# Kernel optimization log

Hardware: AMD Instinct MI355X
Metric: run time of the kernel (lower is better)

Reference implementation:

```python
import jax, jax.numpy as jnp
import numpy as np

NUM_EXPERTS = 64
TOP_K = 2
AUX_COEF = 0.01
Z_COEF = 0.001
INIT_STD = 0.02


def setup_inputs() -> dict:
    key = jax.random.key(0)
    k1, k2 = jax.random.split(key)
    B, S, D = 4, 4096, 2048
    x = jax.random.normal(k1, (B, S, D), dtype=jnp.float32)
    gate_w = jax.random.normal(k2, (NUM_EXPERTS, D), dtype=jnp.float32) * INIT_STD
    return {"x": x, "gate_w": gate_w}


def reference(x, gate_w):
    B, S, D = x.shape
    E, K = NUM_EXPERTS, TOP_K
    # gate linear: (B,S,D) @ (D,E) -> (B,S,E), cast to fp32 like .float()
    logits = jnp.einsum('bsd,ed->bse', x, gate_w).astype(jnp.float32)
    weights = jax.nn.softmax(logits, axis=-1)
    top_weights, top_indices = jax.lax.top_k(weights, K)
    top_weights = top_weights / jnp.sum(top_weights, axis=-1, keepdims=True)
    # load-balance aux loss (training branch)
    flat_idx = top_indices.reshape(-1)
    tokens_per_expert = jax.ops.segment_sum(
        jnp.ones_like(flat_idx, dtype=jnp.float32), flat_idx, num_segments=E)
    f = tokens_per_expert / (B * S * K)
    P = jnp.mean(weights, axis=(0, 1))
    balance_loss = E * jnp.sum(f * P)
    z_loss = jnp.mean(jnp.square(jax.nn.logsumexp(logits, axis=-1)))
    aux_loss = AUX_COEF * balance_loss + Z_COEF * z_loss
    return top_indices, top_weights, aux_loss
```

## Files before the change

### kernel.cpp

```cpp
#include <hip/hip_runtime.h>
#include <math.h>

#define NTOK 16384
#define DDIM 2048
#define NEXP 64
#define NKQ 16
#define KSLICE 128
#define TPB 64

typedef __attribute__((ext_vector_type(8))) short bf16x8;
typedef __attribute__((ext_vector_type(4))) float f32x4;


__device__ __forceinline__ void split3pk(float a, float b,
                                         unsigned &H, unsigned &M, unsigned &L) {
    asm("v_cvt_pk_bf16_f32 %0, %1, %2" : "=v"(H) : "v"(a), "v"(b));
    float ra = a - __builtin_bit_cast(float, H << 16);
    float rb = b - __builtin_bit_cast(float, H & 0xffff0000u);
    asm("v_cvt_pk_bf16_f32 %0, %1, %2" : "=v"(M) : "v"(ra), "v"(rb));
    float sa = ra - __builtin_bit_cast(float, M << 16);
    float sb = rb - __builtin_bit_cast(float, M & 0xffff0000u);
    asm("v_cvt_pk_bf16_f32 %0, %1, %2" : "=v"(L) : "v"(sa), "v"(sb));
}

__device__ __forceinline__ void keepf(float4 &v) {
    asm volatile("" : "+v"(v.x), "+v"(v.y), "+v"(v.z), "+v"(v.w));
}

__global__ void k_wpack(const float* __restrict__ gw, unsigned short* __restrict__ wp,
                        float* __restrict__ aux) {
    if (blockIdx.x == 0 && threadIdx.x < 132) aux[threadIdx.x] = 0.f;
    int idx = blockIdx.x * 256 + threadIdx.x;
    int lane = idx & 63;
    int ks   = (idx >> 6) & 63;
    int eg   = idx >> 12;
    int e  = eg * 16 + (lane & 15);
    int k0 = ks * 32 + (lane >> 4) * 8;
    const float* src = gw + (size_t)e * DDIM + k0;
    uint4 H, M, L;
    split3pk(src[0], src[1], H.x, M.x, L.x);
    split3pk(src[2], src[3], H.y, M.y, L.y);
    split3pk(src[4], src[5], H.z, M.z, L.z);
    split3pk(src[6], src[7], H.w, M.w, L.w);
    size_t fb = ((size_t)ks * 12 + eg * 3) * 512 + lane * 8;
    *(uint4*)(wp + fb)        = H;
    *(uint4*)(wp + fb + 512)  = M;
    *(uint4*)(wp + fb + 1024) = L;
}

__global__ __launch_bounds__(256, 2)
void k_gemm(const float* __restrict__ x, const unsigned short* __restrict__ wp,
            float* __restrict__ part) {
    __shared__ __align__(16) char Ws[49152];

    const int tid  = threadIdx.x;
    const int kq   = blockIdx.x & 15;
    const int tok0 = (blockIdx.x >> 4) * TPB;
    const int lane = tid & 63;
    const int wvu  = __builtin_amdgcn_readfirstlane(tid >> 6);
    const int tau  = lane & 15;
    const int kap  = lane >> 4;

    {
        const char* wsrc = (const char*)wp + (size_t)kq * 49152;
        #pragma unroll
        for (int r = 0; r < 12; ++r) {
            const char* g = wsrc + (size_t)(r * 256 + tid) * 16;
            char* l = Ws + (size_t)(r * 256 + wvu * 64) * 16;
            __builtin_amdgcn_global_load_lds(
                (const __attribute__((address_space(1))) void*)g,
                (__attribute__((address_space(3))) void*)l, 16, 0, 0);
        }
    }

    const float* xb = x + (size_t)(tok0 + wvu * 16 + tau) * DDIM
                        + kq * KSLICE + kap * 8;
    float4 x0a = *(const float4*)(xb);
    float4 x0b = *(const float4*)(xb + 4);
    float4 x1a = *(const float4*)(xb + 32);
    float4 x1b = *(const float4*)(xb + 36);
    float4 x2a = *(const float4*)(xb + 64);
    float4 x2b = *(const float4*)(xb + 68);
    float4 x3a = *(const float4*)(xb + 96);
    float4 x3b = *(const float4*)(xb + 100);
    keepf(x0a); keepf(x0b); keepf(x1a); keepf(x1b);
    keepf(x2a); keepf(x2b); keepf(x3a); keepf(x3b);

    __syncthreads();

    f32x4 acc[4];
    #pragma unroll
    for (int eg = 0; eg < 4; ++eg) acc[eg] = (f32x4){0.f, 0.f, 0.f, 0.f};

    #pragma unroll
    for (int ks = 0; ks < 4; ++ks) {
        float4 a = (ks == 0) ? x0a : (ks == 1) ? x1a : (ks == 2) ? x2a : x3a;
        float4 b = (ks == 0) ? x0b : (ks == 1) ? x1b : (ks == 2) ? x2b : x3b;
        uint4 Ah, Am, Al;
        split3pk(a.x, a.y, Ah.x, Am.x, Al.x);
        split3pk(a.z, a.w, Ah.y, Am.y, Al.y);
        split3pk(b.x, b.y, Ah.z, Am.z, Al.z);
        split3pk(b.z, b.w, Ah.w, Am.w, Al.w);
        bf16x8 Ahv = __builtin_bit_cast(bf16x8, Ah);
        bf16x8 Amv = __builtin_bit_cast(bf16x8, Am);
        bf16x8 Alv = __builtin_bit_cast(bf16x8, Al);

        #pragma unroll
        for (int eg = 0; eg < 4; ++eg) {
            const char* wb = Ws + ks * 12288 + eg * 3072 + lane * 16;
            bf16x8 Bh = *(const bf16x8*)(wb);
            bf16x8 Bm = *(const bf16x8*)(wb + 1024);
            bf16x8 Bl = *(const bf16x8*)(wb + 2048);
            acc[eg] = __builtin_amdgcn_mfma_f32_16x16x32_bf16(Ahv, Bh, acc[eg], 0, 0, 0);
            acc[eg] = __builtin_amdgcn_mfma_f32_16x16x32_bf16(Ahv, Bm, acc[eg], 0, 0, 0);
            acc[eg] = __builtin_amdgcn_mfma_f32_16x16x32_bf16(Amv, Bh, acc[eg], 0, 0, 0);
            acc[eg] = __builtin_amdgcn_mfma_f32_16x16x32_bf16(Ahv, Bl, acc[eg], 0, 0, 0);
            acc[eg] = __builtin_amdgcn_mfma_f32_16x16x32_bf16(Alv, Bh, acc[eg], 0, 0, 0);
            acc[eg] = __builtin_amdgcn_mfma_f32_16x16x32_bf16(Amv, Bm, acc[eg], 0, 0, 0);
        }
    }

    float* pb = part + ((size_t)kq * NTOK + tok0 + wvu * 16) * 64;
    #pragma unroll
    for (int eg = 0; eg < 4; ++eg)
        #pragma unroll
        for (int j = 0; j < 4; ++j)
            pb[(kap * 4 + j) * 64 + eg * 16 + tau] = acc[eg][j];
}

__global__ __launch_bounds__(256, 2)
void k_reduce(const float* __restrict__ part, float* __restrict__ out,
              float* __restrict__ gcnt, float* __restrict__ gP,
              float* __restrict__ gz) {
    __shared__ float Ps[NEXP], Cnt[NEXP], Zs;
    const int tid = threadIdx.x;
    if (tid < NEXP) { Ps[tid] = 0.f; Cnt[tid] = 0.f; }
    if (tid == 0) Zs = 0.f;
    __syncthreads();

    const int lane = tid & 63;
    const int wv   = tid >> 6;
    const int g    = lane >> 4;
    const int s    = lane & 15;
    const int t    = blockIdx.x * 16 + wv * 4 + g;
    const int e4   = s * 4;

    f32x4 a = {0.f, 0.f, 0.f, 0.f};
    #pragma unroll
    for (int q = 0; q < NKQ; ++q) {
        const f32x4 v = *(const f32x4*)(part + ((size_t)q * NTOK + t) * 64 + e4);
        a[0] += v[0]; a[1] += v[1]; a[2] += v[2]; a[3] += v[3];
    }

    float m1 = a[0], m2 = -INFINITY;
    int   i1 = e4,   i2 = NEXP;
    #pragma unroll
    for (int j = 1; j < 4; ++j) {
        float v = a[j]; int idx = e4 + j;
        if (v > m1)      { m2 = m1; i2 = i1; m1 = v; i1 = idx; }
        else if (v > m2) { m2 = v;  i2 = idx; }
    }
    #pragma unroll
    for (int off = 1; off < 16; off <<= 1) {
        float n1 = __shfl_xor(m1, off, 16);
        int   j1 = __shfl_xor(i1, off, 16);
        float n2 = __shfl_xor(m2, off, 16);
        int   j2 = __shfl_xor(i2, off, 16);
        bool pwin = (n1 > m1) || (n1 == m1 && j1 < i1);
        float w1 = pwin ? n1 : m1;  int wi1 = pwin ? j1 : i1;
        float c  = pwin ? m1 : n1;  int ci  = pwin ? i1 : j1;
        float ws = pwin ? n2 : m2;  int wsi = pwin ? j2 : i2;
        bool csec = (c > ws) || (c == ws && ci < wsi);
        m1 = w1; i1 = wi1;
        m2 = csec ? c : ws; i2 = csec ? ci : wsi;
    }

    float ex0 = expf(a[0] - m1), ex1 = expf(a[1] - m1);
    float ex2 = expf(a[2] - m1), ex3 = expf(a[3] - m1);
    float sum = (ex0 + ex1) + (ex2 + ex3);
    #pragma unroll
    for (int off = 1; off < 16; off <<= 1) sum += __shfl_xor(sum, off, 16);

    float inv = 1.f / sum;
    atomicAdd(&Ps[e4 + 0], ex0 * inv);
    atomicAdd(&Ps[e4 + 1], ex1 * inv);
    atomicAdd(&Ps[e4 + 2], ex2 * inv);
    atomicAdd(&Ps[e4 + 3], ex3 * inv);

    if (s == 0) {
        float s2  = expf(m2 - m1);
        float w1v = 1.f / (1.f + s2);
        ((float2*)out)[t]              = make_float2((float)i1, (float)i2);
        ((float2*)(out + 2 * NTOK))[t] = make_float2(w1v, s2 * w1v);
        atomicAdd(&Cnt[i1], 1.f);
        atomicAdd(&Cnt[i2], 1.f);
        float lse = m1 + logf(sum);
        atomicAdd(&Zs, lse * lse);
    }
    __syncthreads();

    if (tid < NEXP) {
        atomicAdd(&gcnt[tid], Cnt[tid]);
        atomicAdd(&gP[tid],   Ps[tid]);
    }
    if (tid == 0) atomicAdd(gz, Zs);
}

__global__ void k_final(const float* __restrict__ ws, float* __restrict__ out) {
    int lane = threadIdx.x;
    float v = ws[lane] * ws[64 + lane];
    #pragma unroll
    for (int off = 32; off > 0; off >>= 1) v += __shfl_xor(v, off);
    if (lane == 0) {
        float bal = 64.f * v / (32768.f * 16384.f);
        float z   = ws[128] / 16384.f;
        out[4 * NTOK] = 0.01f * bal + 0.001f * z;
    }
}

extern "C" void kernel_launch(void* const* d_in, const int* in_sizes, int n_in,
                              void* d_out, int out_size, void* d_ws, size_t ws_size,
                              hipStream_t stream) {
    const float* x  = (const float*)d_in[0];
    const float* gw = (const float*)d_in[1];
    float* out = (float*)d_out;
    float* wsf = (float*)d_ws;
    unsigned short* wp = (unsigned short*)((char*)d_ws + 1024);
    float* part = (float*)((char*)d_ws + (1 << 20));

    k_wpack<<<64, 256, 0, stream>>>(gw, wp, wsf);
    k_gemm<<<NKQ * (NTOK / TPB), 256, 0, stream>>>(x, wp, part);
    k_reduce<<<NTOK / 16, 256, 0, stream>>>(part, out, wsf, wsf + 64, wsf + 128);
    k_final<<<1, 64, 0, stream>>>(wsf, out);
}
```

Measured before the change: 79.15 us.

## Fuse weight packing into GEMM and final loss into reduce kernel

Drops the separate weight-packing kernel. Each GEMM block now loads its fp32 gate-weight slice, splits it into three bf16 parts and writes them straight to LDS. The final aux-loss kernel is folded into the reduce kernel through a last-block-done atomic counter. Together this removes two kernel launches and the packed-weight round trip through global memory, at the cost of every GEMM block redoing the bf16 split on its slice and more VALU work before the MFMA loop.

```diff
diff --git a/kernel.cpp b/kernel.cpp
--- a/kernel.cpp
+++ b/kernel.cpp
@@ -27,30 +27,9 @@
     asm volatile("" : "+v"(v.x), "+v"(v.y), "+v"(v.z), "+v"(v.w));
 }
 
-__global__ void k_wpack(const float* __restrict__ gw, unsigned short* __restrict__ wp,
-                        float* __restrict__ aux) {
-    if (blockIdx.x == 0 && threadIdx.x < 132) aux[threadIdx.x] = 0.f;
-    int idx = blockIdx.x * 256 + threadIdx.x;
-    int lane = idx & 63;
-    int ks   = (idx >> 6) & 63;
-    int eg   = idx >> 12;
-    int e  = eg * 16 + (lane & 15);
-    int k0 = ks * 32 + (lane >> 4) * 8;
-    const float* src = gw + (size_t)e * DDIM + k0;
-    uint4 H, M, L;
-    split3pk(src[0], src[1], H.x, M.x, L.x);
-    split3pk(src[2], src[3], H.y, M.y, L.y);
-    split3pk(src[4], src[5], H.z, M.z, L.z);
-    split3pk(src[6], src[7], H.w, M.w, L.w);
-    size_t fb = ((size_t)ks * 12 + eg * 3) * 512 + lane * 8;
-    *(uint4*)(wp + fb)        = H;
-    *(uint4*)(wp + fb + 512)  = M;
-    *(uint4*)(wp + fb + 1024) = L;
-}
-
 __global__ __launch_bounds__(256, 2)
-void k_gemm(const float* __restrict__ x, const unsigned short* __restrict__ wp,
-            float* __restrict__ part) {
+void k_gemm(const float* __restrict__ x, const float* __restrict__ gw,
+            float* __restrict__ part, float* __restrict__ aux) {
     __shared__ __align__(16) char Ws[49152];
 
     const int tid  = threadIdx.x;
@@ -61,17 +40,7 @@
     const int tau  = lane & 15;
     const int kap  = lane >> 4;
 
-    {
-        const char* wsrc = (const char*)wp + (size_t)kq * 49152;
-        #pragma unroll
-        for (int r = 0; r < 12; ++r) {
-            const char* g = wsrc + (size_t)(r * 256 + tid) * 16;
-            char* l = Ws + (size_t)(r * 256 + wvu * 64) * 16;
-            __builtin_amdgcn_global_load_lds(
-                (const __attribute__((address_space(1))) void*)g,
-                (__attribute__((address_space(3))) void*)l, 16, 0, 0);
-        }
-    }
+    if (blockIdx.x == 0 && tid < 136) aux[tid] = 0.f;
 
     const float* xb = x + (size_t)(tok0 + wvu * 16 + tau) * DDIM
                         + kq * KSLICE + kap * 8;
@@ -83,9 +52,31 @@
     float4 x2b = *(const float4*)(xb + 68);
     float4 x3a = *(const float4*)(xb + 96);
     float4 x3b = *(const float4*)(xb + 100);
+
+    {
+        const int e  = tid >> 2;
+        const int ks = tid & 3;
+        const int eg = e >> 4;
+        const float* gsrc = gw + (size_t)e * DDIM + kq * KSLICE + ks * 32;
+        char* base = Ws + ks * 12288 + eg * 3072;
+        #pragma unroll
+        for (int g = 0; g < 4; ++g) {
+            float4 fa = *(const float4*)(gsrc + g * 8);
+            float4 fb = *(const float4*)(gsrc + g * 8 + 4);
+            uint4 H, M, L;
+            split3pk(fa.x, fa.y, H.x, M.x, L.x);
+            split3pk(fa.z, fa.w, H.y, M.y, L.y);
+            split3pk(fb.x, fb.y, H.z, M.z, L.z);
+            split3pk(fb.z, fb.w, H.w, M.w, L.w);
+            const int lo = (g * 16 + (e & 15)) * 16;
+            *(uint4*)(base + lo)        = H;
+            *(uint4*)(base + 1024 + lo) = M;
+            *(uint4*)(base + 2048 + lo) = L;
+        }
+    }
+
     keepf(x0a); keepf(x0b); keepf(x1a); keepf(x1b);
     keepf(x2a); keepf(x2b); keepf(x3a); keepf(x3b);
-
     __syncthreads();
 
     f32x4 acc[4];
@@ -131,8 +122,9 @@
 __global__ __launch_bounds__(256, 2)
 void k_reduce(const float* __restrict__ part, float* __restrict__ out,
               float* __restrict__ gcnt, float* __restrict__ gP,
-              float* __restrict__ gz) {
+              float* __restrict__ gz, unsigned* __restrict__ ctr) {
     __shared__ float Ps[NEXP], Cnt[NEXP], Zs;
+    __shared__ int lastBlk;
     const int tid = threadIdx.x;
     if (tid < NEXP) { Ps[tid] = 0.f; Cnt[tid] = 0.f; }
     if (tid == 0) Zs = 0.f;
@@ -204,17 +196,25 @@
         atomicAdd(&gP[tid],   Ps[tid]);
     }
     if (tid == 0) atomicAdd(gz, Zs);
-}
-
-__global__ void k_final(const float* __restrict__ ws, float* __restrict__ out) {
-    int lane = threadIdx.x;
-    float v = ws[lane] * ws[64 + lane];
-    #pragma unroll
-    for (int off = 32; off > 0; off >>= 1) v += __shfl_xor(v, off);
-    if (lane == 0) {
-        float bal = 64.f * v / (32768.f * 16384.f);
-        float z   = ws[128] / 16384.f;
-        out[4 * NTOK] = 0.01f * bal + 0.001f * z;
+
+    __syncthreads();
+    if (tid == 0) {
+        __threadfence();
+        unsigned old = atomicAdd(ctr, 1u);
+        lastBlk = (old == gridDim.x - 1);
+    }
+    __syncthreads();
+    if (lastBlk && tid < 64) {
+        float c = atomicAdd(&gcnt[tid], 0.f);
+        float p = atomicAdd(&gP[tid],   0.f);
+        float v = c * p;
+        #pragma unroll
+        for (int off = 32; off > 0; off >>= 1) v += __shfl_xor(v, off);
+        if (tid == 0) {
+            float z = atomicAdd(gz, 0.f);
+            float bal = 64.f * v / (32768.f * 16384.f);
+            out[4 * NTOK] = 0.01f * bal + 0.001f * (z / 16384.f);
+        }
     }
 }
 
@@ -225,11 +225,9 @@
     const float* gw = (const float*)d_in[1];
     float* out = (float*)d_out;
     float* wsf = (float*)d_ws;
-    unsigned short* wp = (unsigned short*)((char*)d_ws + 1024);
     float* part = (float*)((char*)d_ws + (1 << 20));
 
-    k_wpack<<<64, 256, 0, stream>>>(gw, wp, wsf);
-    k_gemm<<<NKQ * (NTOK / TPB), 256, 0, stream>>>(x, wp, part);
-    k_reduce<<<NTOK / 16, 256, 0, stream>>>(part, out, wsf, wsf + 64, wsf + 128);
-    k_final<<<1, 64, 0, stream>>>(wsf, out);
-}
+    k_gemm<<<NKQ * (NTOK / TPB), 256, 0, stream>>>(x, gw, part, wsf);
+    k_reduce<<<NTOK / 16, 256, 0, stream>>>(part, out, wsf, wsf + 64, wsf + 128,
+                                            (unsigned*)(wsf + 132));
+}
```

New measurement: 89.57 us. +13.2%, slower.
